# Performance work log

Hardware: AMD Instinct MI355X
Metric: run time of the kernel (lower is better)

## Reference

```python
import jax, jax.numpy as jnp
import numpy as np

N = 4194304          # total elements
NUM_IDS = 262144     # sorted ids drawn from [0, NUM_IDS)
M_CAP = NUM_IDS + 1  # static upper bound on number of runs (sorted input)
L_CAP = 128          # static upper bound on run length (safe for this distribution)


def setup_inputs() -> dict:
    key = jax.random.key(0)
    k1, k2 = jax.random.split(key)
    ids = jnp.sort(jax.random.randint(k1, (N,), 0, NUM_IDS, dtype=jnp.int32))
    features = jax.random.normal(k2, (N,), dtype=jnp.float32)
    return {"ids": ids, "features": features}


def _group(ids, features):
    """Run-length grouping of consecutive equal ids into a padded [M_CAP, L_CAP] layout.
    Faithful to the tf.scan original: the FINAL run is never emitted (it stays in state).
    Rows beyond the valid runs are zero-filled; their ids are -1 (the original's sentinel).
    """
    n = ids.shape[0]
    ar = jnp.arange(n, dtype=jnp.int32)
    # boundary detection -> run index per element via prefix sum
    is_start = jnp.concatenate([jnp.ones((1,), bool), ids[1:] != ids[:-1]])
    seg = jnp.cumsum(is_start.astype(jnp.int32)) - 1      # [N] run id per element
    num_runs = seg[-1] + 1
    valid_seg = seg < (num_runs - 1)                        # drop last run (scan never emits it)
    # start position of each run (segment-min of element index)
    starts = jnp.full((M_CAP,), n, dtype=jnp.int32).at[seg].min(ar)
    pos = ar - starts[seg]                                  # [N] position within run
    ok = valid_seg & (pos < L_CAP)
    seg_idx = jnp.where(ok, seg, M_CAP)                     # out-of-range -> dropped
    padded = jnp.zeros((M_CAP, L_CAP), features.dtype).at[seg_idx, pos].set(features, mode='drop')
    run_ids = jnp.full((M_CAP,), -1, dtype=ids.dtype).at[jnp.where(valid_seg, seg, M_CAP)].set(ids, mode='drop')
    return run_ids, padded


def reference(ids, features):
    return _group(ids, features)
```

## Files before the change

kernel.cpp:

```cpp
#include <hip/hip_runtime.h>

#define N_ELEM   4194304
#define NUM_IDS  262144
#define M_CAP    (NUM_IDS + 1)
#define L_CAP    128

#define NTILES   1024
#define TILE     4096
#define NTHR     256
#define EPT      16

#define WS_TICKET 0
#define WS_TILES  4

#define ST_SHIFT  30
#define ST_AGG    (1u << ST_SHIFT)
#define ST_PRE    (3u << ST_SHIFT)
#define VAL_MASK  ((1u << ST_SHIFT) - 1u)
#define POISON    0xAAAAAAAAu

#define P_TOTAL   (M_CAP * L_CAP)
#define OUT_TOTAL ((size_t)M_CAP + P_TOTAL)

__global__ void __launch_bounds__(NTHR, 6)
k_fused(const int* __restrict__ ids,
        const float* __restrict__ feat,
        float* __restrict__ out,
        unsigned int* __restrict__ ws) {
    __shared__ int lds_start[TILE + 1];
    __shared__ int smw[4];
    __shared__ int bc[2];

    const int t    = threadIdx.x;
    const int lane = t & 63;
    const int wid  = t >> 6;

    if (t == 0) bc[0] = (int)(atomicAdd(&ws[WS_TICKET], 1u) - POISON);
    __syncthreads();
    const int vt = bc[0];
    const int tile_base = vt * TILE;
    const int tile_end  = tile_base + TILE;
    const int base      = tile_base + t * EPT;

    int v[EPT];
    {
        const int4* p4 = (const int4*)(ids + base);
        int4 a = p4[0], b4 = p4[1], c4 = p4[2], d4 = p4[3];
        v[0]=a.x; v[1]=a.y; v[2]=a.z; v[3]=a.w;
        v[4]=b4.x; v[5]=b4.y; v[6]=b4.z; v[7]=b4.w;
        v[8]=c4.x; v[9]=c4.y; v[10]=c4.z; v[11]=c4.w;
        v[12]=d4.x; v[13]=d4.y; v[14]=d4.z; v[15]=d4.w;
    }
    const int prev = (base == 0) ? -1 : ids[base - 1];

    unsigned flagbits = 0;
    int c = 0;
#pragma unroll
    for (int j = 0; j < EPT; ++j) {
        int f = (v[j] != ((j == 0) ? prev : v[j - 1]));
        flagbits |= ((unsigned)f << j);
        c += f;
    }

    int inc = c;
#pragma unroll
    for (int off = 1; off < 64; off <<= 1) {
        int nb = __shfl_up(inc, off);
        if (lane >= off) inc += nb;
    }
    if (lane == 63) smw[wid] = inc;
    __syncthreads();
    int wbase = 0, tot = 0;
#pragma unroll
    for (int w = 0; w < 4; ++w) {
        int s = smw[w];
        tot += s;
        if (w < wid) wbase += s;
    }
    const int excl = wbase + inc - c;
    const int cnt  = tot;

    if (t == 0) {
        unsigned w = (vt == 0) ? (ST_PRE | (unsigned)cnt) : (ST_AGG | (unsigned)cnt);
        __hip_atomic_store(&ws[WS_TILES + vt], w, __ATOMIC_RELAXED,
                           __HIP_MEMORY_SCOPE_AGENT);
    }

    {
        int r = excl;
#pragma unroll
        for (int j = 0; j < EPT; ++j)
            if (flagbits & (1u << j)) lds_start[r++] = base + j;
    }
    __syncthreads();

    if (wid == 1) {
        if (cnt > 0) {
            int e = tile_end;
            if (vt != NTILES - 1) {
                int s_last = lds_start[cnt - 1];
                if (tile_end - s_last < L_CAP) {
                    int vid = ids[s_last];
                    int m0 = (ids[tile_end + lane]      != vid);
                    int m1 = (ids[tile_end + lane + 64] != vid);
                    unsigned long long b0 = __ballot(m0);
                    unsigned long long b1 = __ballot(m1);
                    int ext;
                    if (b0)      ext = __ffsll(b0) - 1;
                    else if (b1) ext = 64 + __ffsll(b1) - 1;
                    else         ext = 128;
                    e = tile_end + ext;
                }
            }
            if (lane == 0) lds_start[cnt] = e;
        }
    }

    if (wid == 0) {
        int prefix = 0;
        if (vt > 0) {
            int look = vt - 1;
            for (;;) {
                int idx = look - lane;
                unsigned w = ST_PRE;
                if (idx >= 0)
                    w = __hip_atomic_load(&ws[WS_TILES + idx], __ATOMIC_RELAXED,
                                          __HIP_MEMORY_SCOPE_AGENT);
                unsigned st = w >> ST_SHIFT;
                unsigned long long preB = __ballot(st == 3u);
                unsigned long long invB = __ballot((st & 1u) == 0u);
                if (preB) {
                    int lp = __ffsll(preB) - 1;
                    if (!(invB & ((lp > 0) ? ((1ull << lp) - 1ull) : 0ull))) {
                        int contrib = (lane <= lp) ? (int)(w & VAL_MASK) : 0;
                        for (int o = 32; o; o >>= 1) contrib += __shfl_down(contrib, o);
                        prefix += __shfl(contrib, 0);
                        break;
                    }
                } else if (!invB) {
                    int contrib = (int)(w & VAL_MASK);
                    for (int o = 32; o; o >>= 1) contrib += __shfl_down(contrib, o);
                    prefix += __shfl(contrib, 0);
                    look -= 64;
                    continue;
                }
                __builtin_amdgcn_s_sleep(1);
            }
        }
        if (lane == 0) {
            bc[1] = prefix;
            __hip_atomic_store(&ws[WS_TILES + vt],
                               ST_PRE | (unsigned)(prefix + cnt),
                               __ATOMIC_RELAXED, __HIP_MEMORY_SCOPE_AGENT);
        }
    }
    __syncthreads();

    const int prefix = bc[1];
    int cnt_emit = (vt == NTILES - 1) ? cnt - 1 : cnt;
    if (cnt_emit < 0) cnt_emit = 0;

    for (int r = t; r < cnt_emit; r += NTHR)
        out[prefix + r] = (float)ids[lds_start[r]];

    const size_t q_lo = (size_t)M_CAP + (size_t)prefix * L_CAP;
    if (cnt_emit > 0) {
        if (t < 3) {
            int s0 = lds_start[0];
            int L0 = lds_start[1] - s0; if (L0 > L_CAP) L0 = L_CAP;
            out[q_lo + t] = (t < L0) ? feat[s0 + t] : 0.0f;
        }
        if (t == 3) {
            int sL = lds_start[cnt_emit - 1];
            int LL = lds_start[cnt_emit] - sL; if (LL > L_CAP) LL = L_CAP;
            out[q_lo + (size_t)cnt_emit * L_CAP - 1] =
                (LL == L_CAP) ? feat[sL + 127] : 0.0f;
        }
        float* qa = out + q_lo + 3;
        const int nf4 = cnt_emit * 32 - 1;
#pragma unroll 2
        for (int u = t; u < nf4; u += NTHR) {
            const int pl = 3 + 4 * u;
            const int lm = pl >> 7;
            const int c0 = pl & 127;
            int s0 = lds_start[lm];
            int L0 = lds_start[lm + 1] - s0; if (L0 > L_CAP) L0 = L_CAP;
            float4 r;
            if (c0 != 127) {
                r.x = (c0     < L0) ? feat[s0 + c0]     : 0.0f;
                r.y = (c0 + 1 < L0) ? feat[s0 + c0 + 1] : 0.0f;
                r.z = (c0 + 2 < L0) ? feat[s0 + c0 + 2] : 0.0f;
                r.w = (c0 + 3 < L0) ? feat[s0 + c0 + 3] : 0.0f;
            } else {
                int s1 = lds_start[lm + 1];
                int L1 = lds_start[lm + 2] - s1; if (L1 > L_CAP) L1 = L_CAP;
                r.x = (L0 == L_CAP) ? feat[s0 + 127] : 0.0f;
                r.y = (0 < L1) ? feat[s1]     : 0.0f;
                r.z = (1 < L1) ? feat[s1 + 1] : 0.0f;
                r.w = (2 < L1) ? feat[s1 + 2] : 0.0f;
            }
            *(float4*)(qa + 4 * (size_t)u) = r;
        }
    }

    if (vt == NTILES - 1) {
        const int num_valid = prefix + cnt_emit;
        for (int i = num_valid + t; i < M_CAP; i += NTHR)
            out[i] = -1.0f;
        const size_t p0 = (size_t)M_CAP + (size_t)num_valid * L_CAP;
        for (size_t p = p0 + t; p < OUT_TOTAL; p += NTHR)
            out[p] = 0.0f;
    }
}

extern "C" void kernel_launch(void* const* d_in, const int* in_sizes, int n_in,
                              void* d_out, int out_size, void* d_ws, size_t ws_size,
                              hipStream_t stream) {
    const int* ids    = (const int*)d_in[0];
    const float* feat = (const float*)d_in[1];
    float* out        = (float*)d_out;
    unsigned int* ws  = (unsigned int*)d_ws;

    k_fused<<<NTILES, NTHR, 0, stream>>>(ids, feat, out, ws);
}
```

Baseline: 209.8 us.

## Zero-fill padded rows then scatter features directly from register tiles

Halves the tile size (2048 elements, 8 per thread) and raises the occupancy hint. Instead of gathering features per output float4 through LDS run starts, each tile now zero-fills its padded rows and then scatters the features it already holds in registers to row/position slots. A third wavefront writes the tail of a run that spills past the tile end. This replaces indirect gather reads with coalesced feature loads, at the cost of writing most output twice (zeros, then scattered non-coalesced stores) plus an extra barrier.

```diff
diff --git a/kernel.cpp b/kernel.cpp
--- a/kernel.cpp
+++ b/kernel.cpp
@@ -5,10 +5,10 @@
 #define M_CAP    (NUM_IDS + 1)
 #define L_CAP    128
 
-#define NTILES   1024
-#define TILE     4096
+#define NTILES   2048
+#define TILE     2048
 #define NTHR     256
-#define EPT      16
+#define EPT      8
 
 #define WS_TICKET 0
 #define WS_TILES  4
@@ -22,7 +22,7 @@
 #define P_TOTAL   (M_CAP * L_CAP)
 #define OUT_TOTAL ((size_t)M_CAP + P_TOTAL)
 
-__global__ void __launch_bounds__(NTHR, 6)
+__global__ void __launch_bounds__(NTHR, 8)
 k_fused(const int* __restrict__ ids,
         const float* __restrict__ feat,
         float* __restrict__ out,
@@ -45,11 +45,9 @@
     int v[EPT];
     {
         const int4* p4 = (const int4*)(ids + base);
-        int4 a = p4[0], b4 = p4[1], c4 = p4[2], d4 = p4[3];
+        int4 a = p4[0], b4 = p4[1];
         v[0]=a.x; v[1]=a.y; v[2]=a.z; v[3]=a.w;
         v[4]=b4.x; v[5]=b4.y; v[6]=b4.z; v[7]=b4.w;
-        v[8]=c4.x; v[9]=c4.y; v[10]=c4.z; v[11]=c4.w;
-        v[12]=d4.x; v[13]=d4.y; v[14]=d4.z; v[15]=d4.w;
     }
     const int prev = (base == 0) ? -1 : ids[base - 1];
 
@@ -94,26 +92,24 @@
     }
     __syncthreads();
 
-    if (wid == 1) {
-        if (cnt > 0) {
-            int e = tile_end;
-            if (vt != NTILES - 1) {
-                int s_last = lds_start[cnt - 1];
-                if (tile_end - s_last < L_CAP) {
-                    int vid = ids[s_last];
-                    int m0 = (ids[tile_end + lane]      != vid);
-                    int m1 = (ids[tile_end + lane + 64] != vid);
-                    unsigned long long b0 = __ballot(m0);
-                    unsigned long long b1 = __ballot(m1);
-                    int ext;
-                    if (b0)      ext = __ffsll(b0) - 1;
-                    else if (b1) ext = 64 + __ffsll(b1) - 1;
-                    else         ext = 128;
-                    e = tile_end + ext;
-                }
+    if (wid == 1 && cnt > 0) {
+        int e = tile_end;
+        if (vt != NTILES - 1) {
+            int s_last = lds_start[cnt - 1];
+            if (tile_end - s_last < L_CAP) {
+                int vid = ids[s_last];
+                int m0 = (ids[tile_end + lane]      != vid);
+                int m1 = (ids[tile_end + lane + 64] != vid);
+                unsigned long long b0 = __ballot(m0);
+                unsigned long long b1 = __ballot(m1);
+                int ext;
+                if (b0)      ext = __ffsll(b0) - 1;
+                else if (b1) ext = 64 + __ffsll(b1) - 1;
+                else         ext = 128;
+                e = tile_end + ext;
             }
-            if (lane == 0) lds_start[cnt] = e;
-        }
+        }
+        if (lane == 0) lds_start[cnt] = e;
     }
 
     if (wid == 0) {
@@ -157,53 +153,58 @@
     __syncthreads();
 
     const int prefix = bc[1];
-    int cnt_emit = (vt == NTILES - 1) ? cnt - 1 : cnt;
+    const bool last  = (vt == NTILES - 1);
+    int cnt_emit = last ? cnt - 1 : cnt;
     if (cnt_emit < 0) cnt_emit = 0;
-
-    for (int r = t; r < cnt_emit; r += NTHR)
-        out[prefix + r] = (float)ids[lds_start[r]];
 
     const size_t q_lo = (size_t)M_CAP + (size_t)prefix * L_CAP;
     if (cnt_emit > 0) {
-        if (t < 3) {
-            int s0 = lds_start[0];
-            int L0 = lds_start[1] - s0; if (L0 > L_CAP) L0 = L_CAP;
-            out[q_lo + t] = (t < L0) ? feat[s0 + t] : 0.0f;
-        }
-        if (t == 3) {
-            int sL = lds_start[cnt_emit - 1];
-            int LL = lds_start[cnt_emit] - sL; if (LL > L_CAP) LL = L_CAP;
-            out[q_lo + (size_t)cnt_emit * L_CAP - 1] =
-                (LL == L_CAP) ? feat[sL + 127] : 0.0f;
-        }
+        if (t < 3)  out[q_lo + t] = 0.0f;
+        if (t == 3) out[q_lo + (size_t)cnt_emit * L_CAP - 1] = 0.0f;
         float* qa = out + q_lo + 3;
         const int nf4 = cnt_emit * 32 - 1;
-#pragma unroll 2
-        for (int u = t; u < nf4; u += NTHR) {
-            const int pl = 3 + 4 * u;
-            const int lm = pl >> 7;
-            const int c0 = pl & 127;
-            int s0 = lds_start[lm];
-            int L0 = lds_start[lm + 1] - s0; if (L0 > L_CAP) L0 = L_CAP;
-            float4 r;
-            if (c0 != 127) {
-                r.x = (c0     < L0) ? feat[s0 + c0]     : 0.0f;
-                r.y = (c0 + 1 < L0) ? feat[s0 + c0 + 1] : 0.0f;
-                r.z = (c0 + 2 < L0) ? feat[s0 + c0 + 2] : 0.0f;
-                r.w = (c0 + 3 < L0) ? feat[s0 + c0 + 3] : 0.0f;
-            } else {
-                int s1 = lds_start[lm + 1];
-                int L1 = lds_start[lm + 2] - s1; if (L1 > L_CAP) L1 = L_CAP;
-                r.x = (L0 == L_CAP) ? feat[s0 + 127] : 0.0f;
-                r.y = (0 < L1) ? feat[s1]     : 0.0f;
-                r.z = (1 < L1) ? feat[s1 + 1] : 0.0f;
-                r.w = (2 < L1) ? feat[s1 + 2] : 0.0f;
+        const float4 z = {0.0f, 0.0f, 0.0f, 0.0f};
+        for (int u = t; u < nf4; u += NTHR)
+            *(float4*)(qa + 4 * (size_t)u) = z;
+    }
+    __syncthreads();
+
+    {
+        float fv[EPT];
+        const float4* f4 = (const float4*)(feat + base);
+        float4 fa = f4[0], fb = f4[1];
+        fv[0]=fa.x; fv[1]=fa.y; fv[2]=fa.z; fv[3]=fa.w;
+        fv[4]=fb.x; fv[5]=fb.y; fv[6]=fb.z; fv[7]=fb.w;
+
+        int r = excl - 1;
+        int s_cur = (r >= 0) ? lds_start[r] : base - 100000;
+#pragma unroll
+        for (int j = 0; j < EPT; ++j) {
+            if (flagbits & (1u << j)) {
+                ++r; s_cur = base + j;
+                if (!(last && r == cnt - 1))
+                    out[prefix + r] = (float)v[j];
             }
-            *(float4*)(qa + 4 * (size_t)u) = r;
-        }
-    }
-
-    if (vt == NTILES - 1) {
+            int pos = base + j - s_cur;
+            if (pos < L_CAP && r >= 0 && !(last && r == cnt - 1))
+                out[q_lo + (size_t)r * L_CAP + pos] = fv[j];
+        }
+    }
+
+    if (wid == 2 && cnt > 0 && !last) {
+        int s_last = lds_start[cnt - 1];
+        int nExt   = lds_start[cnt] - tile_end;
+        size_t rowb = q_lo + (size_t)(cnt - 1) * L_CAP;
+#pragma unroll
+        for (int p = 0; p < 2; ++p) {
+            int k = lane + 64 * p;
+            int pos = tile_end + k - s_last;
+            if (k < nExt && pos < L_CAP)
+                out[rowb + pos] = feat[tile_end + k];
+        }
+    }
+
+    if (last) {
         const int num_valid = prefix + cnt_emit;
         for (int i = num_valid + t; i < M_CAP; i += NTHR)
             out[i] = -1.0f;
```

After: 199.6 us. 4.9% less time.
